# Optimization experiments

Hardware: AMD Instinct MI355X
Metric: run time of the kernel (lower is better)

Reference implementation:

```python
import jax, jax.numpy as jnp
import numpy as np


def dequant_weight(cb, idx):
    """Reconstruct weight from product-quantization codebooks.
    cb:  [C, K, sub]  codebooks
    idx: [C, out]     int codes per codebook per output row
    returns W: [out, C*sub]
    """
    C = cb.shape[0]
    gathered = cb[jnp.arange(C)[:, None], idx]          # [C, out, sub]
    W = jnp.transpose(gathered, (1, 0, 2))               # [out, C, sub]
    return W.reshape(W.shape[0], -1)                     # [out, C*sub]


def setup_inputs() -> dict:
    key = jax.random.key(0)
    ks = jax.random.split(key, 7)
    B, S, D, H, C, K = 4, 2048, 1024, 4096, 8, 256
    return {
        "x": jax.random.normal(ks[0], (B, S, D), dtype=jnp.float32),
        "cb1": jax.random.normal(ks[1], (C, K, D // C), dtype=jnp.float32) * 0.02,
        "idx1": jax.random.randint(ks[2], (C, H), 0, K, dtype=jnp.int32),
        "b1": jax.random.normal(ks[3], (H,), dtype=jnp.float32) * 0.02,
        "cb2": jax.random.normal(ks[4], (C, K, H // C), dtype=jnp.float32) * 0.02,
        "idx2": jax.random.randint(ks[5], (C, D), 0, K, dtype=jnp.int32),
        "b2": jax.random.normal(ks[6], (D,), dtype=jnp.float32) * 0.02,
    }


def reference(x, cb1, idx1, b1, cb2, idx2, b2):
    # fc1: dequantize W1 [hidden, dim] from shared codebooks, then linear
    W1 = dequant_weight(cb1, idx1)                       # [H, D]
    h = jnp.einsum("bsd,hd->bsh", x, W1) + b1            # [B, S, H]
    h = jax.nn.gelu(h, approximate=False)                # exact GELU (torch default)
    # fc2: dequantize W2 [dim, hidden], linear back to dim
    W2 = dequant_weight(cb2, idx2)                       # [D, H]
    return jnp.einsum("bsh,dh->bsd", h, W2) + b2         # [B, S, D]
```

## Files before the change

kernel.cpp:

```cpp
#include <hip/hip_runtime.h>
#include <hip/hip_bf16.h>
#include <math.h>

typedef __bf16 bf16_t;
typedef bf16_t bf16x8 __attribute__((ext_vector_type(8)));
typedef float f32x4 __attribute__((ext_vector_type(4)));

__device__ __forceinline__ void g2l16(const bf16_t* g, bf16_t* l) {
    __builtin_amdgcn_global_load_lds(
        (const __attribute__((address_space(1))) void*)g,
        (__attribute__((address_space(3))) void*)l, 16, 0, 0);
}

__global__ void prep_all(const void* __restrict__ x,
                         const void* __restrict__ cb1, const int* __restrict__ idx1,
                         const void* __restrict__ b1,
                         const void* __restrict__ cb2, const int* __restrict__ idx2,
                         const void* __restrict__ b2,
                         bf16_t* __restrict__ xb, bf16_t* __restrict__ w1b,
                         bf16_t* __restrict__ w2b, float* __restrict__ b1f,
                         float* __restrict__ b2f, int* __restrict__ flag, int M) {
    __shared__ int s_bad;
    if (threadIdx.x == 0) s_bad = 0;
    __syncthreads();
    const unsigned short* xu = (const unsigned short*)x;
    int cnt = 0;
    for (int i = threadIdx.x; i < 8192; i += 256)
        cnt += (((xu[i] >> 7) & 0xFF) >= 0x88);
#pragma unroll
    for (int o = 32; o > 0; o >>= 1) cnt += __shfl_down(cnt, o, 64);
    if ((threadIdx.x & 63) == 0) atomicAdd(&s_bad, cnt);
    __syncthreads();
    const int f32 = (s_bad > 4);
    if (blockIdx.x == 0 && threadIdx.x == 0) flag[0] = f32;

    const int T0 = (M * 1024) / 8;
    const int T1 = 4096 * 128;
    const int T2 = 1024 * 512;
    const int TB = (4096 + 1024) / 8;
    const int total = T0 + T1 + T2 + TB;
    const int t = blockIdx.x * 256 + threadIdx.x;
    const int stride = gridDim.x * 256;

    for (int i = t; i < total; i += stride) {
        if (i < T0) {
            bf16x8 o;
            if (f32) {
                const float4* p = (const float4*)x;
                float4 a = p[2 * i], b = p[2 * i + 1];
                o[0] = (bf16_t)a.x; o[1] = (bf16_t)a.y; o[2] = (bf16_t)a.z; o[3] = (bf16_t)a.w;
                o[4] = (bf16_t)b.x; o[5] = (bf16_t)b.y; o[6] = (bf16_t)b.z; o[7] = (bf16_t)b.w;
            } else {
                o = ((const bf16x8*)x)[i];
            }
            *(bf16x8*)(xb + (size_t)i * 8) = o;
        } else if (i < T0 + T1 + T2) {
            int g2 = (i >= T0 + T1);
            int ii = g2 ? (i - T0 - T1) : (i - T0);
            int rows = g2 ? 1024 : 4096;
            int logsub = g2 ? 9 : 7;
            int sub = 1 << logsub;
            const int* idx = g2 ? idx2 : idx1;
            const void* cb = g2 ? cb2 : cb1;
            bf16_t* W = g2 ? w2b : w1b;
            int r = ii >> logsub;
            int col = (ii & (sub - 1)) << 3;
            int c = col >> logsub;
            int j = col & (sub - 1);
            int code = idx[c * rows + r];
            size_t src = ((size_t)(c * 256 + code) << logsub) + j;
            bf16x8 o;
            if (f32) {
                const float* s = (const float*)cb + src;
                float4 a = *(const float4*)s;
                float4 b = *(const float4*)(s + 4);
                o[0] = (bf16_t)a.x; o[1] = (bf16_t)a.y; o[2] = (bf16_t)a.z; o[3] = (bf16_t)a.w;
                o[4] = (bf16_t)b.x; o[5] = (bf16_t)b.y; o[6] = (bf16_t)b.z; o[7] = (bf16_t)b.w;
            } else {
                o = *(const bf16x8*)((const bf16_t*)cb + src);
            }
            *(bf16x8*)(W + (size_t)r * ((size_t)sub << 3) + col) = o;
        } else {
            int g = i - (T0 + T1 + T2);
#pragma unroll
            for (int j = 0; j < 8; ++j) {
                int e = g * 8 + j;
                float v;
                const void* src = (e < 4096) ? b1 : b2;
                int k = (e < 4096) ? e : e - 4096;
                v = f32 ? ((const float*)src)[k] : (float)(((const bf16_t*)src)[k]);
                if (e < 4096) b1f[k] = v; else b2f[k] = v;
            }
        }
    }
}

template <bool XCDSW, bool GELU, bool DYNOUT>
__global__ __launch_bounds__(256, 2)
void gemm_bt(const bf16_t* __restrict__ A, const bf16_t* __restrict__ Bw,
             const float* __restrict__ bias,
             bf16_t* __restrict__ obf, float* __restrict__ of32,
             int M, int N, int K, const int* __restrict__ flag) {
    __shared__ __attribute__((aligned(16))) bf16_t sA[128 * 64];
    __shared__ __attribute__((aligned(16))) bf16_t sB[128 * 64];

    const int tid = threadIdx.x;

    int bm, bn;
    if (XCDSW) {
        const int l = blockIdx.y * gridDim.x + blockIdx.x;
        const int xcd = l & 7;
        const int i = l >> 3;
        const int per = gridDim.y >> 3;
        bm = (xcd * per + (i % per)) << 7;
        bn = (i / per) << 7;
    } else {
        bm = blockIdx.y << 7;
        bn = blockIdx.x << 7;
    }

    const int row0 = tid >> 3;
    const int kc0 = ((tid & 7) - row0) & 7;
    const bf16_t* gA = A + (size_t)(bm + row0) * K + kc0 * 8;
    const bf16_t* gB = Bw + (size_t)(bn + row0) * K + kc0 * 8;
    bf16_t* lA = sA + tid * 8;
    bf16_t* lB = sB + tid * 8;
    const size_t pskip = (size_t)32 * K;

    const int lane = tid & 63;
    const int wave = tid >> 6;
    const int quad = lane >> 4;
    const int lr = lane & 15;
    const int wm = (wave & 1) << 6;
    const int wn = (wave >> 1) << 6;

    const int arow = wm + lr;
    const int brow = wn + lr;
    const bf16x8* pA0 = (const bf16x8*)(sA + arow * 64 + ((quad + arow) & 7) * 8);
    const bf16x8* pA1 = (const bf16x8*)(sA + arow * 64 + ((quad + 4 + arow) & 7) * 8);
    const bf16x8* pB0 = (const bf16x8*)(sB + brow * 64 + ((quad + brow) & 7) * 8);
    const bf16x8* pB1 = (const bf16x8*)(sB + brow * 64 + ((quad + 4 + brow) & 7) * 8);

    f32x4 acc[4][4] = {};

    for (int k0 = 0; k0 < K; k0 += 64) {
#pragma unroll
        for (int p = 0; p < 4; ++p) g2l16(gA + p * pskip + k0, lA + p * 2048);
#pragma unroll
        for (int p = 0; p < 4; ++p) g2l16(gB + p * pskip + k0, lB + p * 2048);
        __syncthreads();

        bf16x8 af[4], bf[4];
#pragma unroll
        for (int f = 0; f < 4; ++f) { af[f] = pA0[f * 128]; bf[f] = pB0[f * 128]; }
#pragma unroll
        for (int mi = 0; mi < 4; ++mi)
#pragma unroll
            for (int ni = 0; ni < 4; ++ni)
                acc[mi][ni] = __builtin_amdgcn_mfma_f32_16x16x32_bf16(
                    af[mi], bf[ni], acc[mi][ni], 0, 0, 0);
#pragma unroll
        for (int f = 0; f < 4; ++f) { af[f] = pA1[f * 128]; bf[f] = pB1[f * 128]; }
#pragma unroll
        for (int mi = 0; mi < 4; ++mi)
#pragma unroll
            for (int ni = 0; ni < 4; ++ni)
                acc[mi][ni] = __builtin_amdgcn_mfma_f32_16x16x32_bf16(
                    af[mi], bf[ni], acc[mi][ni], 0, 0, 0);
        __syncthreads();
    }

    const int outf32 = DYNOUT ? *flag : 0;
#pragma unroll
    for (int mi = 0; mi < 4; ++mi) {
#pragma unroll
        for (int ni = 0; ni < 4; ++ni) {
            const int n = bn + wn + ni * 16 + lr;
            const float bs = bias[n];
            f32x4 v = acc[mi][ni];
#pragma unroll
            for (int r = 0; r < 4; ++r) {
                const int m = bm + wm + mi * 16 + quad * 4 + r;
                float val = v[r] + bs;
                if (GELU) val = 0.5f * val * (1.0f + erff(val * 0.70710678118654752f));
                const size_t o = (size_t)m * N + n;
                if (DYNOUT) {
                    if (outf32) of32[o] = val;
                    else        obf[o] = (bf16_t)val;
                } else {
                    obf[o] = (bf16_t)val;
                }
            }
        }
    }
}

extern "C" void kernel_launch(void* const* d_in, const int* in_sizes, int n_in,
                              void* d_out, int out_size, void* d_ws, size_t ws_size,
                              hipStream_t stream) {
    const void* x   = d_in[0];
    const void* cb1 = d_in[1];
    const int*  idx1 = (const int*)d_in[2];
    const void* b1  = d_in[3];
    const void* cb2 = d_in[4];
    const int*  idx2 = (const int*)d_in[5];
    const void* b2  = d_in[6];

    const int D = 1024, H = 4096;
    const int M = in_sizes[0] / D;

    char* ws = (char*)d_ws;
    bf16_t* xb  = (bf16_t*)ws;
    bf16_t* w1b = (bf16_t*)(ws + (size_t)M * D * 2);
    bf16_t* hb  = (bf16_t*)((char*)w1b + (size_t)H * D * 2);
    bf16_t* w2b = (bf16_t*)((char*)hb + (size_t)M * H * 2);
    float*  b1f = (float*)((char*)w2b + (size_t)D * H * 2);
    float*  b2f = b1f + H;
    int*    flag = (int*)(b2f + D);

    prep_all<<<2048, 256, 0, stream>>>(x, cb1, idx1, b1, cb2, idx2, b2,
                                       xb, w1b, w2b, b1f, b2f, flag, M);

    dim3 g1(H / 128, M / 128);
    gemm_bt<false, true, false><<<g1, 256, 0, stream>>>(xb, w1b, b1f, hb, nullptr, M, H, D, flag);

    dim3 g2(D / 128, M / 128);
    gemm_bt<true, false, true><<<g2, 256, 0, stream>>>(hb, w2b, b2f, (bf16_t*)d_out, (float*)d_out, M, D, H, flag);
}
```

Baseline: 249.6 us.

## Use 256x256 double-buffered pipelined GEMM kernel for fc1

```diff
diff --git a/kernel.cpp b/kernel.cpp
--- a/kernel.cpp
+++ b/kernel.cpp
@@ -195,6 +195,179 @@
     }
 }
 
+template <bool GELU, bool DYNOUT>
+__global__ __launch_bounds__(512, 2)
+void gemm256(const bf16_t* __restrict__ A, const bf16_t* __restrict__ Bw,
+             const float* __restrict__ bias,
+             bf16_t* __restrict__ obf, float* __restrict__ of32,
+             int M, int N, int K, const int* __restrict__ flag) {
+    __shared__ __attribute__((aligned(16))) bf16_t sA[2 * 256 * 64];
+    __shared__ __attribute__((aligned(16))) bf16_t sB[2 * 256 * 64];
+
+    const int tid = threadIdx.x;
+    const int NT = K >> 6;
+
+    const int l = blockIdx.x;
+    const int nbm = M >> 8;
+    const int per = nbm >> 3;
+    const int xcd = l & 7;
+    const int i = l >> 3;
+    const int bm = (xcd * per + (i % per)) << 8;
+    const int bn = (i / per) << 8;
+
+    const int row0 = tid >> 3;
+    const int kc = ((tid & 7) - row0) & 7;
+    const bf16_t* gA0 = A + (size_t)(bm + row0) * K + kc * 8;
+    const bf16_t* gB0 = Bw + (size_t)(bn + row0) * K + kc * 8;
+    bf16_t* lA0 = sA + tid * 8;
+    bf16_t* lB0 = sB + tid * 8;
+
+#define STAGE_A(off_, h_, kt_) do {                                   \
+    const bf16_t* g_ = gA0 + (size_t)((h_) * 128) * K + (kt_) * 64;   \
+    bf16_t* l_ = lA0 + (off_) + (h_) * 8192;                          \
+    g2l16(g_, l_);                                                    \
+    g2l16(g_ + (size_t)64 * K, l_ + 4096);                            \
+} while (0)
+#define STAGE_B(off_, h_, kt_) do {                                   \
+    const bf16_t* g_ = gB0 + (size_t)((h_) * 128) * K + (kt_) * 64;   \
+    bf16_t* l_ = lB0 + (off_) + (h_) * 8192;                          \
+    g2l16(g_, l_);                                                    \
+    g2l16(g_ + (size_t)64 * K, l_ + 4096);                            \
+} while (0)
+
+    const int lane = tid & 63;
+    const int wave = tid >> 6;
+    const int wm = wave >> 2;
+    const int wn = wave & 3;
+    const int lr = lane & 15;
+    const int quad = lane >> 4;
+    const int c0 = ((quad + lr) & 7) * 8;
+    const int c1 = ((quad + lr + 4) & 7) * 8;
+    const bf16_t* pA = sA + (wm * 128 + lr) * 64;
+    const bf16_t* pB = sB + (wn * 64 + lr) * 64;
+
+    f32x4 acc[8][4] = {};
+    bf16x8 afr[8][2], bfr[2][2];
+
+    STAGE_A(0, 0, 0); STAGE_A(0, 1, 0); STAGE_B(0, 0, 0); STAGE_B(0, 1, 0);
+    if (NT > 1) { STAGE_A(16384, 0, 1); STAGE_A(16384, 1, 1); STAGE_B(16384, 0, 1); }
+    asm volatile("s_waitcnt vmcnt(6)" ::: "memory");
+    __builtin_amdgcn_s_barrier();
+
+    for (int t = 0; t < NT; ++t) {
+        const int bo = (t & 1) << 14;
+        const int obo = bo ^ 16384;
+
+#pragma unroll
+        for (int mi = 0; mi < 8; ++mi) {
+            afr[mi][0] = *(const bf16x8*)(pA + bo + mi * 1024 + c0);
+            afr[mi][1] = *(const bf16x8*)(pA + bo + mi * 1024 + c1);
+        }
+#pragma unroll
+        for (int j = 0; j < 2; ++j) {
+            bfr[j][0] = *(const bf16x8*)(pB + bo + j * 1024 + c0);
+            bfr[j][1] = *(const bf16x8*)(pB + bo + j * 1024 + c1);
+        }
+        if (t + 1 < NT) STAGE_B(obo, 1, t + 1);
+        __builtin_amdgcn_s_barrier();
+        asm volatile("s_waitcnt lgkmcnt(0)");
+        __builtin_amdgcn_s_setprio(1);
+#pragma unroll
+        for (int mi = 0; mi < 4; ++mi)
+#pragma unroll
+            for (int j = 0; j < 2; ++j) {
+                acc[mi][j] = __builtin_amdgcn_mfma_f32_16x16x32_bf16(
+                    afr[mi][0], bfr[j][0], acc[mi][j], 0, 0, 0);
+                acc[mi][j] = __builtin_amdgcn_mfma_f32_16x16x32_bf16(
+                    afr[mi][1], bfr[j][1], acc[mi][j], 0, 0, 0);
+            }
+        __builtin_amdgcn_s_setprio(0);
+        __builtin_amdgcn_s_barrier();
+
+        if (t + 2 < NT) STAGE_A(bo, 0, t + 2);
+        __builtin_amdgcn_s_barrier();
+        __builtin_amdgcn_s_setprio(1);
+#pragma unroll
+        for (int mi = 4; mi < 8; ++mi)
+#pragma unroll
+            for (int j = 0; j < 2; ++j) {
+                acc[mi][j] = __builtin_amdgcn_mfma_f32_16x16x32_bf16(
+                    afr[mi][0], bfr[j][0], acc[mi][j], 0, 0, 0);
+                acc[mi][j] = __builtin_amdgcn_mfma_f32_16x16x32_bf16(
+                    afr[mi][1], bfr[j][1], acc[mi][j], 0, 0, 0);
+            }
+        __builtin_amdgcn_s_setprio(0);
+        __builtin_amdgcn_s_barrier();
+
+#pragma unroll
+        for (int j = 0; j < 2; ++j) {
+            bfr[j][0] = *(const bf16x8*)(pB + bo + (2 + j) * 1024 + c0);
+            bfr[j][1] = *(const bf16x8*)(pB + bo + (2 + j) * 1024 + c1);
+        }
+        if (t + 2 < NT) STAGE_A(bo, 1, t + 2);
+        __builtin_amdgcn_s_barrier();
+        asm volatile("s_waitcnt lgkmcnt(0)");
+        __builtin_amdgcn_s_setprio(1);
+#pragma unroll
+        for (int mi = 4; mi < 8; ++mi)
+#pragma unroll
+            for (int j = 0; j < 2; ++j) {
+                acc[mi][2 + j] = __builtin_amdgcn_mfma_f32_16x16x32_bf16(
+                    afr[mi][0], bfr[j][0], acc[mi][2 + j], 0, 0, 0);
+                acc[mi][2 + j] = __builtin_amdgcn_mfma_f32_16x16x32_bf16(
+                    afr[mi][1], bfr[j][1], acc[mi][2 + j], 0, 0, 0);
+            }
+        __builtin_amdgcn_s_setprio(0);
+        __builtin_amdgcn_s_barrier();
+
+        if (t + 2 < NT) STAGE_B(bo, 0, t + 2);
+        __builtin_amdgcn_s_barrier();
+        __builtin_amdgcn_s_setprio(1);
+#pragma unroll
+        for (int mi = 0; mi < 4; ++mi)
+#pragma unroll
+            for (int j = 0; j < 2; ++j) {
+                acc[mi][2 + j] = __builtin_amdgcn_mfma_f32_16x16x32_bf16(
+                    afr[mi][0], bfr[j][0], acc[mi][2 + j], 0, 0, 0);
+                acc[mi][2 + j] = __builtin_amdgcn_mfma_f32_16x16x32_bf16(
+                    afr[mi][1], bfr[j][1], acc[mi][2 + j], 0, 0, 0);
+            }
+        __builtin_amdgcn_s_setprio(0);
+        if (t + 2 < NT) asm volatile("s_waitcnt vmcnt(6)" ::: "memory");
+        else            asm volatile("s_waitcnt vmcnt(0)" ::: "memory");
+        __builtin_amdgcn_s_barrier();
+    }
+
+#undef STAGE_A
+#undef STAGE_B
+
+    const int outf32 = DYNOUT ? *flag : 0;
+    const int mrow = bm + wm * 128 + quad * 4;
+    const int ncol = bn + wn * 64 + lr;
+#pragma unroll
+    for (int mi = 0; mi < 8; ++mi) {
+#pragma unroll
+        for (int j = 0; j < 4; ++j) {
+            const int n = ncol + j * 16;
+            const float bs = bias[n];
+            f32x4 v = acc[mi][j];
+#pragma unroll
+            for (int r = 0; r < 4; ++r) {
+                const int m = mrow + mi * 16 + r;
+                float val = v[r] + bs;
+                if (GELU) val = 0.5f * val * (1.0f + erff(val * 0.70710678118654752f));
+                const size_t o = (size_t)m * N + n;
+                if (DYNOUT) {
+                    if (outf32) of32[o] = val;
+                    else        obf[o] = (bf16_t)val;
+                } else {
+                    obf[o] = (bf16_t)val;
+                }
+            }
+        }
+    }
+}
+
 extern "C" void kernel_launch(void* const* d_in, const int* in_sizes, int n_in,
                               void* d_out, int out_size, void* d_ws, size_t ws_size,
                               hipStream_t stream) {
@@ -221,9 +394,10 @@
     prep_all<<<2048, 256, 0, stream>>>(x, cb1, idx1, b1, cb2, idx2, b2,
                                        xb, w1b, w2b, b1f, b2f, flag, M);
 
-    dim3 g1(H / 128, M / 128);
-    gemm_bt<false, true, false><<<g1, 256, 0, stream>>>(xb, w1b, b1f, hb, nullptr, M, H, D, flag);
+    gemm256<true, false><<<(M / 256) * (H / 256), 512, 0, stream>>>(
+        xb, w1b, b1f, hb, nullptr, M, H, D, flag);
 
     dim3 g2(D / 128, M / 128);
-    gemm_bt<true, false, true><<<g2, 256, 0, stream>>>(hb, w2b, b2f, (bf16_t*)d_out, (float*)d_out, M, D, H, flag);
+    gemm_bt<true, false, true><<<g2, 256, 0, stream>>>(hb, w2b, b2f,
+        (bf16_t*)d_out, (float*)d_out, M, D, H, flag);
 }
```

New measurement: 267.2 us. 7.1% more time.
